# Optimization experiments

Measured on AMD Instinct MI355X. Metric: run time of the kernel, lower is better.

## Reference

```python
import jax, jax.numpy as jnp
import numpy as np

TOP_K = 2


def setup_inputs() -> dict:
    key = jax.random.key(0)
    k1, k2, k3, k4 = jax.random.split(key, 4)
    B, S, H, I, E = 2, 1024, 2048, 1408, 8
    hidden_states = jax.random.normal(k1, (B, S, H), dtype=jnp.float32)
    gate_w = jax.random.normal(k2, (E, H), dtype=jnp.float32) * (1.0 / np.sqrt(H))
    # stacked expert weights: gate_up_proj [E, 2I, H], down_proj [E, H, I] (torch Linear [out,in])
    w1 = jax.random.normal(k3, (E, 2 * I, H), dtype=jnp.float32) * (1.0 / np.sqrt(H))
    w2 = jax.random.normal(k4, (E, H, I), dtype=jnp.float32) * (1.0 / np.sqrt(I))
    return {"hidden_states": hidden_states, "gate_w": gate_w, "w1": w1, "w2": w2}


def reference(hidden_states, gate_w, w1, w2):
    B, S, H = hidden_states.shape
    E = gate_w.shape[0]
    T = B * S
    x = hidden_states.reshape(T, H)

    # --- gating: softmax -> top-k -> renormalize ---
    logits = jnp.einsum('th,eh->te', x, gate_w)            # [T, E]
    probs = jax.nn.softmax(logits, axis=-1)
    topw, sel = jax.lax.top_k(probs, TOP_K)                # [T, K]
    topw = topw / jnp.sum(topw, axis=-1, keepdims=True)

    # combine weights: [T, E], zero for unselected experts (equivalent to
    # dispatch/permute + per-token routing-weight scale + unpermute + sum)
    combine = jnp.zeros((T, E), dtype=x.dtype).at[
        jnp.arange(T)[:, None], sel].add(topw)

    # --- grouped expert FFN (computed densely per expert) ---
    gate_up = jnp.einsum('th,eoh->eto', x, w1)             # [E, T, 2I]
    g, u = jnp.split(gate_up, 2, axis=-1)
    act = jax.nn.silu(g) * u                               # SiluAndMul, [E, T, I]
    expert_out = jnp.einsum('eti,ehi->eth', act, w2)       # [E, T, H]

    # --- combine ---
    out = jnp.einsum('eth,te->th', expert_out, combine)    # [T, H]
    return out.reshape(B, S, H)
```

## Files before the change

### kernel.cpp

```cpp
#include <hip/hip_runtime.h>
#include <hip/hip_bf16.h>
#include <math.h>

#define T_TOK 2048
#define H_DIM 2048
#define I_DIM 1408
#define E_NUM 8
#define I2    2816

typedef __attribute__((ext_vector_type(8))) short short8;
typedef __attribute__((ext_vector_type(4))) float floatx4;
typedef __attribute__((ext_vector_type(8))) unsigned short bf16x8;
typedef __attribute__((ext_vector_type(4))) unsigned short bf16x4;
typedef unsigned short u16;

__device__ __forceinline__ u16 f2bf(float x) {
    unsigned u = __builtin_bit_cast(unsigned, x);
    return (u16)((u + 0x7FFFu + ((u >> 16) & 1u)) >> 16);
}

__device__ __forceinline__ bf16x8 pack8(float4 a, float4 b) {
    bf16x8 o;
    o[0] = f2bf(a.x); o[1] = f2bf(a.y); o[2] = f2bf(a.z); o[3] = f2bf(a.w);
    o[4] = f2bf(b.x); o[5] = f2bf(b.y); o[6] = f2bf(b.z); o[7] = f2bf(b.w);
    return o;
}

__device__ __forceinline__ floatx4 mfma16(short8 a, short8 b, floatx4 c) {
    return __builtin_amdgcn_mfma_f32_16x16x32_bf16(a, b, c, 0, 0, 0);
}

__device__ __forceinline__ void gload16(const u16* g, u16* l) {
    __builtin_amdgcn_global_load_lds(
        (const __attribute__((address_space(1))) unsigned int*)g,
        (__attribute__((address_space(3))) unsigned int*)l, 16, 0, 0);
}

__global__ void moe_gating(const float* __restrict__ x, const float* __restrict__ gw,
                           u16* __restrict__ xb, float* __restrict__ wts,
                           int* __restrict__ counts, int* __restrict__ entries) {
    const int lane = threadIdx.x & 63;
    const int wv   = threadIdx.x >> 6;
    const int t    = blockIdx.x * 4 + wv;
    float acc[E_NUM];
#pragma unroll
    for (int e = 0; e < E_NUM; ++e) acc[e] = 0.f;
    const float4* xr = (const float4*)(x + (size_t)t * H_DIM);
    u16* xo = xb + (size_t)t * H_DIM;
#pragma unroll
    for (int j = 0; j < 8; ++j) {
        float4 xv = xr[lane + 64 * j];
        bf16x4 xw;
        xw[0] = f2bf(xv.x); xw[1] = f2bf(xv.y); xw[2] = f2bf(xv.z); xw[3] = f2bf(xv.w);
        *(bf16x4*)(xo + (lane + 64 * j) * 4) = xw;
#pragma unroll
        for (int e = 0; e < E_NUM; ++e) {
            float4 g = ((const float4*)(gw + (size_t)e * H_DIM))[lane + 64 * j];
            acc[e] += xv.x * g.x + xv.y * g.y + xv.z * g.z + xv.w * g.w;
        }
    }
#pragma unroll
    for (int off = 32; off > 0; off >>= 1)
#pragma unroll
        for (int e = 0; e < E_NUM; ++e) acc[e] += __shfl_xor(acc[e], off, 64);

    if (lane == 0) {
        int a = 0; float la = acc[0];
        for (int e = 1; e < E_NUM; ++e) if (acc[e] > la) { la = acc[e]; a = e; }
        int b = (a == 0) ? 1 : 0; float lb = acc[b];
        for (int e = 0; e < E_NUM; ++e)
            if (e != a && acc[e] > lb) { lb = acc[e]; b = e; }
        float wa = 1.f / (1.f + expf(lb - la));
        wts[t * 2 + 0] = wa;
        wts[t * 2 + 1] = 1.f - wa;
        int p0 = atomicAdd(&counts[a], 1); entries[a * T_TOK + p0] = t * 2;
        int p1 = atomicAdd(&counts[b], 1); entries[b * T_TOK + p1] = t * 2 + 1;
    }
}

__global__ __launch_bounds__(256)
void cvt_bf16(const float* __restrict__ src, u16* __restrict__ dst, long n8) {
    const float4* s4 = (const float4*)src;
    const long stride = (long)gridDim.x * 256;
    for (long i = (long)blockIdx.x * 256 + threadIdx.x; i < n8; i += stride) {
        float4 a = s4[2 * i], b = s4[2 * i + 1];
        *(bf16x8*)(dst + (size_t)i * 8) = pack8(a, b);
    }
}

__global__ __launch_bounds__(256)
void moe_mfma1_pre(const u16* __restrict__ xb, const u16* __restrict__ w1b,
                   const int* __restrict__ counts, const int* __restrict__ entries,
                   u16* __restrict__ act) {
    const int bid = blockIdx.x;
    const int e   = bid & 7;
    const int rem = bid >> 3;
    const int tn  = rem >> 4;
    const int tm  = rem & 15;
    const int ne  = counts[e];
    if (tm * 128 >= ne) return;

    __shared__ __align__(16) u16 As[128 * 64];
    __shared__ __align__(16) u16 Bg[64 * 64];
    __shared__ __align__(16) u16 Bu[64 * 64];
    __shared__ int rowv[128];

    const int tid = threadIdx.x;
    if (tid < 128) {
        int r = tm * 128 + tid;
        rowv[tid] = (r < ne) ? entries[(size_t)e * T_TOK + r] : -1;
    }
    __syncthreads();

    const u16* asrc[4]; int ad[4];
#pragma unroll
    for (int q = 0; q < 4; ++q) {
        int i = q * 256 + tid;
        int row = i >> 3, pc = i & 7;
        int lc = pc ^ (row & 7);
        int v = rowv[row];
        int tok = (v < 0) ? 0 : (v >> 1);
        asrc[q] = xb + (size_t)tok * H_DIM + lc * 8;
        ad[q] = i * 8;
    }
    const u16* gsrc[2]; const u16* usrc[2]; int bd2[2];
#pragma unroll
    for (int q = 0; q < 2; ++q) {
        int i = q * 256 + tid;
        int row = i >> 3, pc = i & 7;
        int lc = pc ^ (row & 7);
        size_t off = ((size_t)e * I2 + tn * 64 + row) * H_DIM + lc * 8;
        gsrc[q] = w1b + off;
        usrc[q] = w1b + off + (size_t)I_DIM * H_DIM;
        bd2[q] = i * 8;
    }

    const int lane = tid & 63, wid = tid >> 6;
    const int wm = wid & 1, wn = wid >> 1;

    floatx4 accG[4][2], accU[4][2];
    const floatx4 z4 = {0.f, 0.f, 0.f, 0.f};
#pragma unroll
    for (int mi = 0; mi < 4; ++mi)
#pragma unroll
        for (int ni = 0; ni < 2; ++ni) { accG[mi][ni] = z4; accU[mi][ni] = z4; }

    int aoff[4][2], boff[2][2];
#pragma unroll
    for (int mi = 0; mi < 4; ++mi) {
        int m = wm * 64 + mi * 16 + (lane & 15);
#pragma unroll
        for (int kk = 0; kk < 2; ++kk)
            aoff[mi][kk] = m * 64 + (((kk * 4 + (lane >> 4)) ^ (m & 7)) * 8);
    }
#pragma unroll
    for (int ni = 0; ni < 2; ++ni) {
        int n = wn * 32 + ni * 16 + (lane & 15);
#pragma unroll
        for (int kk = 0; kk < 2; ++kk)
            boff[ni][kk] = n * 64 + (((kk * 4 + (lane >> 4)) ^ (n & 7)) * 8);
    }

#pragma unroll 1
    for (int k0 = 0; k0 < H_DIM; k0 += 64) {
#pragma unroll
        for (int q = 0; q < 4; ++q) gload16(asrc[q] + k0, As + ad[q]);
#pragma unroll
        for (int q = 0; q < 2; ++q) {
            gload16(gsrc[q] + k0, Bg + bd2[q]);
            gload16(usrc[q] + k0, Bu + bd2[q]);
        }
        __syncthreads();
#pragma unroll
        for (int kk = 0; kk < 2; ++kk) {
            short8 a[4], g2[2], u2[2];
#pragma unroll
            for (int mi = 0; mi < 4; ++mi) a[mi] = *(const short8*)(As + aoff[mi][kk]);
#pragma unroll
            for (int ni = 0; ni < 2; ++ni) {
                g2[ni] = *(const short8*)(Bg + boff[ni][kk]);
                u2[ni] = *(const short8*)(Bu + boff[ni][kk]);
            }
#pragma unroll
            for (int mi = 0; mi < 4; ++mi)
#pragma unroll
                for (int ni = 0; ni < 2; ++ni) {
                    accG[mi][ni] = mfma16(a[mi], g2[ni], accG[mi][ni]);
                    accU[mi][ni] = mfma16(a[mi], u2[ni], accU[mi][ni]);
                }
        }
        __syncthreads();
    }

    const int obase = tn * 64 + wn * 32;
#pragma unroll
    for (int mi = 0; mi < 4; ++mi)
#pragma unroll
        for (int ni = 0; ni < 2; ++ni)
#pragma unroll
            for (int r = 0; r < 4; ++r) {
                int row = wm * 64 + mi * 16 + (lane >> 4) * 4 + r;
                int v = rowv[row];
                if (v < 0) continue;
                float g = accG[mi][ni][r], u = accU[mi][ni][r];
                float s = g / (1.f + expf(-g)) * u;
                act[(size_t)v * I_DIM + obase + ni * 16 + (lane & 15)] = f2bf(s);
            }
}

__global__ __launch_bounds__(256)
void moe_mfma2_pre(const u16* __restrict__ act, const u16* __restrict__ w2b,
                   const int* __restrict__ counts, const int* __restrict__ entries,
                   const float* __restrict__ wts, float* __restrict__ slot) {
    const int bid = blockIdx.x;
    const int e   = bid & 7;
    const int rem = bid >> 3;
    const int tn  = rem >> 4;
    const int tm  = rem & 15;
    const int ne  = counts[e];
    if (tm * 128 >= ne) return;

    __shared__ __align__(16) u16 As[128 * 64];
    __shared__ __align__(16) u16 Bs[128 * 64];
    __shared__ int   rowv[128];
    __shared__ float roww[128];

    const int tid = threadIdx.x;
    if (tid < 128) {
        int r = tm * 128 + tid;
        int v = (r < ne) ? entries[(size_t)e * T_TOK + r] : -1;
        rowv[tid] = v;
        roww[tid] = (v < 0) ? 0.f : wts[v];
    }
    __syncthreads();

    const u16* asrc[4]; const u16* bsrc[4]; int ad[4];
#pragma unroll
    for (int q = 0; q < 4; ++q) {
        int i = q * 256 + tid;
        int row = i >> 3, pc = i & 7;
        int lc = pc ^ (row & 7);
        int v = rowv[row]; if (v < 0) v = 0;
        asrc[q] = act + (size_t)v * I_DIM + lc * 8;
        bsrc[q] = w2b + ((size_t)e * H_DIM + tn * 128 + row) * I_DIM + lc * 8;
        ad[q] = i * 8;
    }

    const int lane = tid & 63, wid = tid >> 6;
    const int wm = wid & 1, wn = wid >> 1;

    floatx4 acc[4][4];
    const floatx4 z4 = {0.f, 0.f, 0.f, 0.f};
#pragma unroll
    for (int mi = 0; mi < 4; ++mi)
#pragma unroll
        for (int ni = 0; ni < 4; ++ni) acc[mi][ni] = z4;

    int aoff[4][2], boff[4][2];
#pragma unroll
    for (int mi = 0; mi < 4; ++mi) {
        int m = wm * 64 + mi * 16 + (lane & 15);
#pragma unroll
        for (int kk = 0; kk < 2; ++kk)
            aoff[mi][kk] = m * 64 + (((kk * 4 + (lane >> 4)) ^ (m & 7)) * 8);
    }
#pragma unroll
    for (int ni = 0; ni < 4; ++ni) {
        int n = wn * 64 + ni * 16 + (lane & 15);
#pragma unroll
        for (int kk = 0; kk < 2; ++kk)
            boff[ni][kk] = n * 64 + (((kk * 4 + (lane >> 4)) ^ (n & 7)) * 8);
    }

#pragma unroll 1
    for (int k0 = 0; k0 < I_DIM; k0 += 64) {
#pragma unroll
        for (int q = 0; q < 4; ++q) {
            gload16(asrc[q] + k0, As + ad[q]);
            gload16(bsrc[q] + k0, Bs + ad[q]);
        }
        __syncthreads();
#pragma unroll
        for (int kk = 0; kk < 2; ++kk) {
            short8 a[4], b[4];
#pragma unroll
            for (int mi = 0; mi < 4; ++mi) a[mi] = *(const short8*)(As + aoff[mi][kk]);
#pragma unroll
            for (int ni = 0; ni < 4; ++ni) b[ni] = *(const short8*)(Bs + boff[ni][kk]);
#pragma unroll
            for (int mi = 0; mi < 4; ++mi)
#pragma unroll
                for (int ni = 0; ni < 4; ++ni)
                    acc[mi][ni] = mfma16(a[mi], b[ni], acc[mi][ni]);
        }
        __syncthreads();
    }

    const int hbase = tn * 128 + wn * 64;
#pragma unroll
    for (int mi = 0; mi < 4; ++mi)
#pragma unroll
        for (int ni = 0; ni < 4; ++ni)
#pragma unroll
            for (int r = 0; r < 4; ++r) {
                int row = wm * 64 + mi * 16 + (lane >> 4) * 4 + r;
                int v = rowv[row];
                if (v < 0) continue;
                slot[(size_t)v * H_DIM + hbase + ni * 16 + (lane & 15)] =
                    roww[row] * acc[mi][ni][r];
            }
}

__global__ __launch_bounds__(256)
void moe_combine(const float* __restrict__ slot, float* __restrict__ out) {
    int i = blockIdx.x * 256 + threadIdx.x;
    int t = i >> 9, c = i & 511;
    const float4* s4 = (const float4*)slot;
    float4 a = s4[(size_t)(2 * t) * 512 + c];
    float4 b = s4[(size_t)(2 * t + 1) * 512 + c];
    float4 o; o.x = a.x + b.x; o.y = a.y + b.y; o.z = a.z + b.z; o.w = a.w + b.w;
    ((float4*)out)[i] = o;
}

__global__ __launch_bounds__(256)
void moe_mfma1_f32(const u16* __restrict__ xb, const float* __restrict__ w1,
                   const int* __restrict__ counts, const int* __restrict__ entries,
                   u16* __restrict__ act) {
    const int bid = blockIdx.x;
    const int e   = bid & 7;
    const int rem = bid >> 3;
    const int tn  = rem >> 4;
    const int tm  = rem & 15;
    const int ne  = counts[e];
    if (tm * 128 >= ne) return;

    __shared__ __align__(16) u16 As[128 * 64];
    __shared__ __align__(16) u16 Bg[64 * 64];
    __shared__ __align__(16) u16 Bu[64 * 64];
    __shared__ int rowv[128];

    const int tid = threadIdx.x;
    if (tid < 128) {
        int r = tm * 128 + tid;
        rowv[tid] = (r < ne) ? entries[(size_t)e * T_TOK + r] : -1;
    }
    __syncthreads();

    const u16* asrc[4]; int ad[4];
#pragma unroll
    for (int q = 0; q < 4; ++q) {
        int i = q * 256 + tid;
        int row = i >> 3, pc = i & 7;
        int lc = pc ^ (row & 7);
        int v = rowv[row];
        int tok = (v < 0) ? 0 : (v >> 1);
        asrc[q] = xb + (size_t)tok * H_DIM + lc * 8;
        ad[q] = i * 8;
    }
    const int brow = tid >> 2;
    const int bc16 = (tid & 3) * 16;
    const float* gsrc = w1 + ((size_t)e * I2 + tn * 64 + brow) * H_DIM + bc16;
    const float* usrc = gsrc + (size_t)I_DIM * H_DIM;
    const int lc0 = (tid & 3) * 2;
    u16* bgd0 = Bg + brow * 64 + ((lc0    ) ^ (brow & 7)) * 8;
    u16* bgd1 = Bg + brow * 64 + ((lc0 + 1) ^ (brow & 7)) * 8;
    u16* bud0 = Bu + brow * 64 + ((lc0    ) ^ (brow & 7)) * 8;
    u16* bud1 = Bu + brow * 64 + ((lc0 + 1) ^ (brow & 7)) * 8;

    const int lane = tid & 63, wid = tid >> 6;
    const int wm = wid & 1, wn = wid >> 1;

    floatx4 accG[4][2], accU[4][2];
    const floatx4 z4 = {0.f, 0.f, 0.f, 0.f};
#pragma unroll
    for (int mi = 0; mi < 4; ++mi)
#pragma unroll
        for (int ni = 0; ni < 2; ++ni) { accG[mi][ni] = z4; accU[mi][ni] = z4; }

    int aoff[4][2], boff[2][2];
#pragma unroll
    for (int mi = 0; mi < 4; ++mi) {
        int m = wm * 64 + mi * 16 + (lane & 15);
#pragma unroll
        for (int kk = 0; kk < 2; ++kk)
            aoff[mi][kk] = m * 64 + (((kk * 4 + (lane >> 4)) ^ (m & 7)) * 8);
    }
#pragma unroll
    for (int ni = 0; ni < 2; ++ni) {
        int n = wn * 32 + ni * 16 + (lane & 15);
#pragma unroll
        for (int kk = 0; kk < 2; ++kk)
            boff[ni][kk] = n * 64 + (((kk * 4 + (lane >> 4)) ^ (n & 7)) * 8);
    }

#pragma unroll 1
    for (int k0 = 0; k0 < H_DIM; k0 += 64) {
#pragma unroll
        for (int q = 0; q < 4; ++q) gload16(asrc[q] + k0, As + ad[q]);
        {
            const float4* g4 = (const float4*)(gsrc + k0);
            const float4* u4 = (const float4*)(usrc + k0);
            float4 a0 = g4[0], a1 = g4[1], a2 = g4[2], a3 = g4[3];
            float4 b0 = u4[0], b1 = u4[1], b2 = u4[2], b3 = u4[3];
            *(bf16x8*)bgd0 = pack8(a0, a1);
            *(bf16x8*)bgd1 = pack8(a2, a3);
            *(bf16x8*)bud0 = pack8(b0, b1);
            *(bf16x8*)bud1 = pack8(b2, b3);
        }
        __syncthreads();
#pragma unroll
        for (int kk = 0; kk < 2; ++kk) {
            short8 a[4], g2[2], u2[2];
#pragma unroll
            for (int mi = 0; mi < 4; ++mi) a[mi] = *(const short8*)(As + aoff[mi][kk]);
#pragma unroll
            for (int ni = 0; ni < 2; ++ni) {
                g2[ni] = *(const short8*)(Bg + boff[ni][kk]);
                u2[ni] = *(const short8*)(Bu + boff[ni][kk]);
            }
#pragma unroll
            for (int mi = 0; mi < 4; ++mi)
#pragma unroll
                for (int ni = 0; ni < 2; ++ni) {
                    accG[mi][ni] = mfma16(a[mi], g2[ni], accG[mi][ni]);
                    accU[mi][ni] = mfma16(a[mi], u2[ni], accU[mi][ni]);
                }
        }
        __syncthreads();
    }

    const int obase = tn * 64 + wn * 32;
#pragma unroll
    for (int mi = 0; mi < 4; ++mi)
#pragma unroll
        for (int ni = 0; ni < 2; ++ni)
#pragma unroll
            for (int r = 0; r < 4; ++r) {
                int row = wm * 64 + mi * 16 + (lane >> 4) * 4 + r;
                int v = rowv[row];
                if (v < 0) continue;
                float g = accG[mi][ni][r], u = accU[mi][ni][r];
                float s = g / (1.f + expf(-g)) * u;
                act[(size_t)v * I_DIM + obase + ni * 16 + (lane & 15)] = f2bf(s);
            }
}

__global__ __launch_bounds__(256)
void moe_mfma2_f32(const u16* __restrict__ act, const float* __restrict__ w2,
                   const int* __restrict__ counts, const int* __restrict__ entries,
                   const float* __restrict__ wts, float* __restrict__ out) {
    const int bid = blockIdx.x;
    const int e   = bid & 7;
    const int rem = bid >> 3;
    const int tn  = rem >> 4;
    const int tm  = rem & 15;
    const int ne  = counts[e];
    if (tm * 128 >= ne) return;

    __shared__ __align__(16) u16 As[128 * 64];
    __shared__ __align__(16) u16 Bs[128 * 64];
    __shared__ int   rowv[128];
    __shared__ int   rowt[128];
    __shared__ float roww[128];

    const int tid = threadIdx.x;
    if (tid < 128) {
        int r = tm * 128 + tid;
        int v = (r < ne) ? entries[(size_t)e * T_TOK + r] : -1;
        rowv[tid] = v;
        rowt[tid] = (v < 0) ? 0 : (v >> 1);
        roww[tid] = (v < 0) ? 0.f : wts[v];
    }
    __syncthreads();

    const u16* asrc[4]; int ad[4];
#pragma unroll
    for (int q = 0; q < 4; ++q) {
        int i = q * 256 + tid;
        int row = i >> 3, pc = i & 7;
        int lc = pc ^ (row & 7);
        int v = rowv[row]; if (v < 0) v = 0;
        asrc[q] = act + (size_t)v * I_DIM + lc * 8;
        ad[q] = i * 8;
    }
    const int brow = tid >> 1;
    const int bc32 = (tid & 1) * 32;
    const float* bsrc = w2 + ((size_t)e * H_DIM + tn * 128 + brow) * I_DIM + bc32;
    const int lcb = (tid & 1) * 4;
    u16* bd[4];
#pragma unroll
    for (int j = 0; j < 4; ++j)
        bd[j] = Bs + brow * 64 + (((lcb + j) ^ (brow & 7)) * 8);

    const int lane = tid & 63, wid = tid >> 6;
    const int wm = wid & 1, wn = wid >> 1;

    floatx4 acc[4][4];
    const floatx4 z4 = {0.f, 0.f, 0.f, 0.f};
#pragma unroll
    for (int mi = 0; mi < 4; ++mi)
#pragma unroll
        for (int ni = 0; ni < 4; ++ni) acc[mi][ni] = z4;

    int aoff[4][2], boff[4][2];
#pragma unroll
    for (int mi = 0; mi < 4; ++mi) {
        int m = wm * 64 + mi * 16 + (lane & 15);
#pragma unroll
        for (int kk = 0; kk < 2; ++kk)
            aoff[mi][kk] = m * 64 + (((kk * 4 + (lane >> 4)) ^ (m & 7)) * 8);
    }
#pragma unroll
    for (int ni = 0; ni < 4; ++ni) {
        int n = wn * 64 + ni * 16 + (lane & 15);
#pragma unroll
        for (int kk = 0; kk < 2; ++kk)
            boff[ni][kk] = n * 64 + (((kk * 4 + (lane >> 4)) ^ (n & 7)) * 8);
    }

#pragma unroll 1
    for (int k0 = 0; k0 < I_DIM; k0 += 64) {
#pragma unroll
        for (int q = 0; q < 4; ++q) gload16(asrc[q] + k0, As + ad[q]);
        {
            const float4* b4 = (const float4*)(bsrc + k0);
            float4 t0 = b4[0], t1 = b4[1], t2 = b4[2], t3 = b4[3];
            float4 t4 = b4[4], t5 = b4[5], t6 = b4[6], t7 = b4[7];
            *(bf16x8*)bd[0] = pack8(t0, t1);
            *(bf16x8*)bd[1] = pack8(t2, t3);
            *(bf16x8*)bd[2] = pack8(t4, t5);
            *(bf16x8*)bd[3] = pack8(t6, t7);
        }
        __syncthreads();
#pragma unroll
        for (int kk = 0; kk < 2; ++kk) {
            short8 a[4], b[4];
#pragma unroll
            for (int mi = 0; mi < 4; ++mi) a[mi] = *(const short8*)(As + aoff[mi][kk]);
#pragma unroll
            for (int ni = 0; ni < 4; ++ni) b[ni] = *(const short8*)(Bs + boff[ni][kk]);
#pragma unroll
            for (int mi = 0; mi < 4; ++mi)
#pragma unroll
                for (int ni = 0; ni < 4; ++ni)
                    acc[mi][ni] = mfma16(a[mi], b[ni], acc[mi][ni]);
        }
        __syncthreads();
    }

    const int hbase = tn * 128 + wn * 64;
#pragma unroll
    for (int mi = 0; mi < 4; ++mi)
#pragma unroll
        for (int ni = 0; ni < 4; ++ni)
#pragma unroll
            for (int r = 0; r < 4; ++r) {
                int row = wm * 64 + mi * 16 + (lane >> 4) * 4 + r;
                if (rowv[row] < 0) continue;
                atomicAdd(out + (size_t)rowt[row] * H_DIM + hbase + ni * 16 + (lane & 15),
                          roww[row] * acc[mi][ni][r]);
            }
}

extern "C" void kernel_launch(void* const* d_in, const int* in_sizes, int n_in,
                              void* d_out, int out_size, void* d_ws, size_t ws_size,
                              hipStream_t stream) {
    const float* x  = (const float*)d_in[0];
    const float* gw = (const float*)d_in[1];
    const float* w1 = (const float*)d_in[2];
    const float* w2 = (const float*)d_in[3];
    float* out = (float*)d_out;

    char* ws = (char*)d_ws;
    int*   counts  = (int*)ws;
    int*   entries = (int*)(ws + 256);
    float* wts     = (float*)(ws + 256 + 65536);
    u16* xb  = (u16*)(ws + 131072);
    u16* act = xb  + (size_t)T_TOK * H_DIM;
    u16* w1b = act + (size_t)2 * T_TOK * I_DIM;
    u16* w2b = w1b + (size_t)E_NUM * I2 * H_DIM;
    float* slot = (float*)w1b;

    const size_t need = 131072 + 2ull * ((size_t)T_TOK * H_DIM + 2ull * T_TOK * I_DIM +
                                         (size_t)E_NUM * I2 * H_DIM +
                                         (size_t)E_NUM * H_DIM * I_DIM);
    const bool pre = (ws_size >= need);

    (void)hipMemsetAsync(counts, 0, 256, stream);

    moe_gating<<<T_TOK / 4, 256, 0, stream>>>(x, gw, xb, wts, counts, entries);

    if (pre) {
        cvt_bf16<<<4096, 256, 0, stream>>>(w1, w1b, (long)E_NUM * I2 * H_DIM / 8);
        cvt_bf16<<<4096, 256, 0, stream>>>(w2, w2b, (long)E_NUM * H_DIM * I_DIM / 8);
        moe_mfma1_pre<<<22 * 16 * E_NUM, 256, 0, stream>>>(xb, w1b, counts, entries, act);
        moe_mfma2_pre<<<16 * 16 * E_NUM, 256, 0, stream>>>(act, w2b, counts, entries, wts, slot);
        moe_combine<<<T_TOK * H_DIM / 4 / 256, 256, 0, stream>>>(slot, out);
    } else {
        (void)hipMemsetAsync(out, 0, (size_t)T_TOK * H_DIM * sizeof(float), stream);
        moe_mfma1_f32<<<22 * 16 * E_NUM, 256, 0, stream>>>(xb, w1, counts, entries, act);
        moe_mfma2_f32<<<16 * 16 * E_NUM, 256, 0, stream>>>(act, w2, counts, entries, wts, out);
    }
}
```

Baseline: 568.0 us.

## Double-buffer LDS tiles in expert GEMMs and merge weight conversion kernels

Both grouped expert GEMM kernels now use two LDS buffers. The next K-tile is loaded while the current tile is computed, with one barrier per iteration instead of two, to hide global-load latency behind MFMA work. The two fp32-to-bf16 weight conversion launches are merged into one kernel to save a launch and the tail between them. Doubled LDS use (up to 64KB per block in the second GEMM) may lower occupancy.

```diff
diff --git a/kernel.cpp b/kernel.cpp
--- a/kernel.cpp
+++ b/kernel.cpp
@@ -79,12 +79,17 @@
 }
 
 __global__ __launch_bounds__(256)
-void cvt_bf16(const float* __restrict__ src, u16* __restrict__ dst, long n8) {
-    const float4* s4 = (const float4*)src;
+void cvt_both(const float* __restrict__ w1, const float* __restrict__ w2,
+              u16* __restrict__ w1b, u16* __restrict__ w2b) {
+    const long n1 = (long)E_NUM * I2 * H_DIM / 8;
+    const long n2 = (long)E_NUM * H_DIM * I_DIM / 8;
     const long stride = (long)gridDim.x * 256;
-    for (long i = (long)blockIdx.x * 256 + threadIdx.x; i < n8; i += stride) {
-        float4 a = s4[2 * i], b = s4[2 * i + 1];
-        *(bf16x8*)(dst + (size_t)i * 8) = pack8(a, b);
+    for (long i = (long)blockIdx.x * 256 + threadIdx.x; i < n1 + n2; i += stride) {
+        const float4* s4; u16* dst; long j;
+        if (i < n1) { s4 = (const float4*)w1; dst = w1b; j = i; }
+        else        { s4 = (const float4*)w2; dst = w2b; j = i - n1; }
+        float4 a = s4[2 * j], b = s4[2 * j + 1];
+        *(bf16x8*)(dst + (size_t)j * 8) = pack8(a, b);
     }
 }
 
@@ -100,9 +105,9 @@
     const int ne  = counts[e];
     if (tm * 128 >= ne) return;
 
-    __shared__ __align__(16) u16 As[128 * 64];
-    __shared__ __align__(16) u16 Bg[64 * 64];
-    __shared__ __align__(16) u16 Bu[64 * 64];
+    __shared__ __align__(16) u16 As[2][128 * 64];
+    __shared__ __align__(16) u16 Bg[2][64 * 64];
+    __shared__ __align__(16) u16 Bu[2][64 * 64];
     __shared__ int rowv[128];
 
     const int tid = threadIdx.x;
@@ -161,25 +166,25 @@
             boff[ni][kk] = n * 64 + (((kk * 4 + (lane >> 4)) ^ (n & 7)) * 8);
     }
 
-#pragma unroll 1
-    for (int k0 = 0; k0 < H_DIM; k0 += 64) {
-#pragma unroll
-        for (int q = 0; q < 4; ++q) gload16(asrc[q] + k0, As + ad[q]);
+    auto stage = [&](int B, int k0) {
+#pragma unroll
+        for (int q = 0; q < 4; ++q) gload16(asrc[q] + k0, &As[B][ad[q]]);
 #pragma unroll
         for (int q = 0; q < 2; ++q) {
-            gload16(gsrc[q] + k0, Bg + bd2[q]);
-            gload16(usrc[q] + k0, Bu + bd2[q]);
-        }
-        __syncthreads();
+            gload16(gsrc[q] + k0, &Bg[B][bd2[q]]);
+            gload16(usrc[q] + k0, &Bu[B][bd2[q]]);
+        }
+    };
+    auto compute = [&](int B) {
 #pragma unroll
         for (int kk = 0; kk < 2; ++kk) {
             short8 a[4], g2[2], u2[2];
 #pragma unroll
-            for (int mi = 0; mi < 4; ++mi) a[mi] = *(const short8*)(As + aoff[mi][kk]);
+            for (int mi = 0; mi < 4; ++mi) a[mi] = *(const short8*)(&As[B][aoff[mi][kk]]);
 #pragma unroll
             for (int ni = 0; ni < 2; ++ni) {
-                g2[ni] = *(const short8*)(Bg + boff[ni][kk]);
-                u2[ni] = *(const short8*)(Bu + boff[ni][kk]);
+                g2[ni] = *(const short8*)(&Bg[B][boff[ni][kk]]);
+                u2[ni] = *(const short8*)(&Bu[B][boff[ni][kk]]);
             }
 #pragma unroll
             for (int mi = 0; mi < 4; ++mi)
@@ -189,8 +194,19 @@
                     accU[mi][ni] = mfma16(a[mi], u2[ni], accU[mi][ni]);
                 }
         }
+    };
+
+    stage(0, 0);
+    __syncthreads();
+    int cur = 0;
+#pragma unroll 1
+    for (int k0 = 64; k0 < H_DIM; k0 += 64) {
+        stage(cur ^ 1, k0);
+        compute(cur);
         __syncthreads();
-    }
+        cur ^= 1;
+    }
+    compute(cur);
 
     const int obase = tn * 64 + wn * 32;
 #pragma unroll
@@ -220,8 +236,8 @@
     const int ne  = counts[e];
     if (tm * 128 >= ne) return;
 
-    __shared__ __align__(16) u16 As[128 * 64];
-    __shared__ __align__(16) u16 Bs[128 * 64];
+    __shared__ __align__(16) u16 As[2][128 * 64];
+    __shared__ __align__(16) u16 Bs[2][128 * 64];
     __shared__ int   rowv[128];
     __shared__ float roww[128];
 
@@ -272,29 +288,40 @@
             boff[ni][kk] = n * 64 + (((kk * 4 + (lane >> 4)) ^ (n & 7)) * 8);
     }
 
-#pragma unroll 1
-    for (int k0 = 0; k0 < I_DIM; k0 += 64) {
+    auto stage = [&](int B, int k0) {
 #pragma unroll
         for (int q = 0; q < 4; ++q) {
-            gload16(asrc[q] + k0, As + ad[q]);
-            gload16(bsrc[q] + k0, Bs + ad[q]);
-        }
-        __syncthreads();
+            gload16(asrc[q] + k0, &As[B][ad[q]]);
+            gload16(bsrc[q] + k0, &Bs[B][ad[q]]);
+        }
+    };
+    auto compute = [&](int B) {
 #pragma unroll
         for (int kk = 0; kk < 2; ++kk) {
             short8 a[4], b[4];
 #pragma unroll
-            for (int mi = 0; mi < 4; ++mi) a[mi] = *(const short8*)(As + aoff[mi][kk]);
-#pragma unroll
-            for (int ni = 0; ni < 4; ++ni) b[ni] = *(const short8*)(Bs + boff[ni][kk]);
+            for (int mi = 0; mi < 4; ++mi) a[mi] = *(const short8*)(&As[B][aoff[mi][kk]]);
+#pragma unroll
+            for (int ni = 0; ni < 4; ++ni) b[ni] = *(const short8*)(&Bs[B][boff[ni][kk]]);
 #pragma unroll
             for (int mi = 0; mi < 4; ++mi)
 #pragma unroll
                 for (int ni = 0; ni < 4; ++ni)
                     acc[mi][ni] = mfma16(a[mi], b[ni], acc[mi][ni]);
         }
+    };
+
+    stage(0, 0);
+    __syncthreads();
+    int cur = 0;
+#pragma unroll 1
+    for (int k0 = 64; k0 < I_DIM; k0 += 64) {
+        stage(cur ^ 1, k0);
+        compute(cur);
         __syncthreads();
-    }
+        cur ^= 1;
+    }
+    compute(cur);
 
     const int hbase = tn * 128 + wn * 64;
 #pragma unroll
@@ -591,8 +618,7 @@
     moe_gating<<<T_TOK / 4, 256, 0, stream>>>(x, gw, xb, wts, counts, entries);
 
     if (pre) {
-        cvt_bf16<<<4096, 256, 0, stream>>>(w1, w1b, (long)E_NUM * I2 * H_DIM / 8);
-        cvt_bf16<<<4096, 256, 0, stream>>>(w2, w2b, (long)E_NUM * H_DIM * I_DIM / 8);
+        cvt_both<<<4096, 256, 0, stream>>>(w1, w2, w1b, w2b);
         moe_mfma1_pre<<<22 * 16 * E_NUM, 256, 0, stream>>>(xb, w1b, counts, entries, act);
         moe_mfma2_pre<<<16 * 16 * E_NUM, 256, 0, stream>>>(act, w2b, counts, entries, wts, slot);
         moe_combine<<<T_TOK * H_DIM / 4 / 256, 256, 0, stream>>>(slot, out);
```

Result: slower. 659.3 us (+16.1%).
